# Optimization experiments

Hardware: AMD Instinct MI355X
Metric: run time of the kernel (lower is better)

## Reference

```python
import jax, jax.numpy as jnp
import numpy as np

B, S, QD, KD, VD, OD = 8, 2048, 768, 768, 768, 512

def setup_inputs() -> dict:
    key = jax.random.key(0)
    ks = jax.random.split(key, 14)
    s_q = 1.0 / np.sqrt(QD)
    s_k = 1.0 / np.sqrt(KD)
    s_v = 1.0 / np.sqrt(VD)
    return {
        "query": jax.random.normal(ks[0], (B, S, QD), jnp.float32),
        "key": jax.random.normal(ks[1], (B, S, KD), jnp.float32),
        "value": jax.random.normal(ks[2], (B, S, VD), jnp.float32),
        "Wqr": jax.random.normal(ks[3], (QD, OD), jnp.float32) * s_q,
        "bqr": jnp.zeros((OD,), jnp.float32),
        "Wqi": jax.random.normal(ks[4], (QD, OD), jnp.float32) * s_q,
        "bqi": jnp.zeros((OD,), jnp.float32),
        "Wkr": jax.random.normal(ks[5], (KD, OD), jnp.float32) * s_k,
        "bkr": jnp.zeros((OD,), jnp.float32),
        "Wki": jax.random.normal(ks[6], (KD, OD), jnp.float32) * s_k,
        "bki": jnp.zeros((OD,), jnp.float32),
        "Wv": jax.random.normal(ks[7], (VD, OD), jnp.float32) * s_v,
        "bv": jnp.zeros((OD,), jnp.float32),
        "coherence_weight": jnp.asarray(1.0, jnp.float32),
    }

def reference(query, key, value, Wqr, bqr, Wqi, bqi, Wkr, bkr, Wki, bki, Wv, bv, coherence_weight):
    # Complex-valued projections (real/imag parts via separate linears)
    q_r = jnp.einsum("bsq,qo->bso", query, Wqr) + bqr
    q_i = jnp.einsum("bsq,qo->bso", query, Wqi) + bqi
    k_r = jnp.einsum("bsk,ko->bso", key, Wkr) + bkr
    k_i = jnp.einsum("bsk,ko->bso", key, Wki) + bki
    v = jnp.einsum("bsv,vo->bso", value, Wv) + bv
    # Complex QK^T: (q_r + i q_i)(k_r - i k_i)^T pieces, as in the torch code
    att_real = jnp.einsum("bso,bto->bst", q_r, k_r) + jnp.einsum("bso,bto->bst", q_i, k_i)
    att_imag = jnp.einsum("bso,bto->bst", q_i, k_r) - jnp.einsum("bso,bto->bst", q_r, k_i)
    att_mag = jnp.sqrt(att_real ** 2 + att_imag ** 2)
    scale = jnp.asarray(1.0 / np.sqrt(OD), att_mag.dtype)
    weights = jax.nn.softmax(att_mag * scale, axis=-1)  # [B,S,S]
    output = jnp.einsum("bst,bto->bso", weights, v)  # [B,S,OD]
    coherence = jnp.mean(att_imag ** 2) * coherence_weight
    return output, coherence
```

## Files before the change

kernel.cpp:

```cpp
#include <hip/hip_runtime.h>
#include <math.h>
#include <stdint.h>

#define S_    2048
#define SCALE_ 0.044194173824159216f

typedef __attribute__((ext_vector_type(8))) short short8;
typedef __attribute__((ext_vector_type(4))) float f32x4;

#define MFMA16(a, b, c) __builtin_amdgcn_mfma_f32_16x16x32_bf16((a), (b), (c), 0, 0, 0)

__device__ __forceinline__ void glds16(const void* g, void* l) {
  __builtin_amdgcn_global_load_lds(
      (const __attribute__((address_space(1))) void*)g,
      (__attribute__((address_space(3))) void*)l, 16, 0, 0);
}

__device__ __forceinline__ unsigned short f2bf(float f) {
  unsigned u = __float_as_uint(f);
  u += 0x7FFFu + ((u >> 16) & 1u);
  return (unsigned short)(u >> 16);
}

__global__ __launch_bounds__(256) void convert3_kernel(
    const float* __restrict__ a, const float* __restrict__ b,
    const float* __restrict__ c, unsigned short* __restrict__ oa,
    unsigned short* __restrict__ ob, unsigned short* __restrict__ oc) {
  int i = blockIdx.x * 256 + threadIdx.x;
  int which = i / 3145728;
  int off = i - which * 3145728;
  const float* s = (which == 0) ? a : (which == 1) ? b : c;
  unsigned short* d = (which == 0) ? oa : (which == 1) ? ob : oc;
  float4 v = ((const float4*)s)[off];
  ushort4 o;
  o.x = f2bf(v.x); o.y = f2bf(v.y); o.z = f2bf(v.z); o.w = f2bf(v.w);
  ((ushort4*)d)[off] = o;
}

__global__ void bias_build_kernel(const float* bqr, const float* bqi,
                                  const float* bkr, const float* bki,
                                  const float* bv, float* bq, float* bk,
                                  float* bvo) {
  int t = blockIdx.x * 256 + threadIdx.x;
  if (t < 512) { bq[t] = bqr[t]; bk[t] = bkr[t]; bvo[t] = bv[t]; }
  else if (t < 1024) { bq[t] = bqi[t - 512]; bk[t] = bki[t - 512]; }
}

__global__ __launch_bounds__(256) void wtrans_kernel(
    const float* __restrict__ W, unsigned short* __restrict__ Wt, int N,
    int row_off) {
  __shared__ float t[32][33];
  int n0 = blockIdx.x * 32, k0 = blockIdx.y * 32;
  int tx = threadIdx.x & 31, ty = threadIdx.x >> 5;
#pragma unroll
  for (int r = 0; r < 4; ++r)
    t[ty + r * 8][tx] = W[(size_t)(k0 + ty + r * 8) * N + n0 + tx];
  __syncthreads();
#pragma unroll
  for (int r = 0; r < 4; ++r)
    Wt[(size_t)(row_off + n0 + ty + r * 8) * 768 + k0 + tx] =
        f2bf(t[tx][ty + r * 8]);
}

__global__ void init_kernel(float* lsum, float* coh) {
  int t = blockIdx.x * 256 + threadIdx.x;
  if (t < 16384) lsum[t] = 0.f;
  if (t == 0) *coh = 0.f;
}

__global__ __launch_bounds__(256, 2) void proj_kernel(
    const unsigned short* __restrict__ Xb, const unsigned short* __restrict__ Wt,
    const float* __restrict__ bias, unsigned short* __restrict__ Y, int N,
    int vt_mode) {
  __shared__ char lds[32768];
  const int tid = threadIdx.x;
  const int lane = tid & 63, wid = tid >> 6;
  const int wi = wid >> 1, wj = wid & 1;
  const int m0 = blockIdx.y * 128, n0 = blockIdx.x * 128;
  const char* Xc = (const char*)Xb;
  const char* Wc = (const char*)Wt;

  f32x4 acc[4][4] = {};
  const int tile = wid >> 1;

  for (int s = 0; s < 12; ++s) {
    __syncthreads();
#pragma unroll
    for (int iss = 0; iss < 8; ++iss) {
      int gbase = wid * 512 + iss * 64;
      int loc = (gbase & 1023) + lane;
      int r = loc >> 3, blk = loc & 7;
      int sb = blk ^ (r & 7);
      const char* src = (tile == 0)
          ? Xc + (size_t)(m0 + r) * 1536 + s * 128 + sb * 16
          : Wc + (size_t)(n0 + r) * 1536 + s * 128 + sb * 16;
      glds16(src, lds + gbase * 16);
    }
    __syncthreads();
#pragma unroll
    for (int kk = 0; kk < 2; ++kk) {
      int blk = kk * 4 + (lane >> 4);
      short8 a[4];
#pragma unroll
      for (int i = 0; i < 4; ++i) {
        int row = wi * 64 + i * 16 + (lane & 15);
        a[i] = *(const short8*)(lds + row * 128 + ((blk ^ (row & 7)) << 4));
      }
#pragma unroll
      for (int j = 0; j < 4; ++j) {
        int row = wj * 64 + j * 16 + (lane & 15);
        short8 b = *(const short8*)(lds + 16384 + row * 128 +
                                    ((blk ^ (row & 7)) << 4));
#pragma unroll
        for (int i = 0; i < 4; ++i) acc[i][j] = MFMA16(a[i], b, acc[i][j]);
      }
    }
  }

#pragma unroll
  for (int j = 0; j < 4; ++j) {
    int n = n0 + wj * 64 + j * 16 + (lane & 15);
    float bn = bias[n];
    if (!vt_mode) {
#pragma unroll
      for (int i = 0; i < 4; ++i) {
        int mrow = m0 + wi * 64 + i * 16 + (lane >> 4) * 4;
#pragma unroll
        for (int r = 0; r < 4; ++r)
          Y[(size_t)(mrow + r) * N + n] = f2bf(acc[i][j][r] + bn);
      }
    } else {
#pragma unroll
      for (int i = 0; i < 4; ++i) {
        int mrow = m0 + wi * 64 + i * 16 + (lane >> 4) * 4;
        int b = mrow >> 11, key = mrow & 2047;
        ushort4 o;
        o.x = f2bf(acc[i][j][0] + bn);
        o.y = f2bf(acc[i][j][1] + bn);
        o.z = f2bf(acc[i][j][2] + bn);
        o.w = f2bf(acc[i][j][3] + bn);
        *(ushort4*)&Y[((size_t)b * 512 + n) * 2048 + key] = o;
      }
    }
  }
}

__global__ __launch_bounds__(512, 2) void score_kernel(
    const unsigned short* __restrict__ Qcat,
    const unsigned short* __restrict__ Kcat, unsigned short* __restrict__ P,
    float* __restrict__ lsum, float* __restrict__ coh) {
  __shared__ char lds[147456];
  const int tid = threadIdx.x;
  const int lane = tid & 63, wid = tid >> 6;
  const int wm = wid >> 1;
  const int wn = wid & 1;
  const int lr = lane & 15;
  const int lk = lane >> 4;
  const int l8 = lane >> 3, lb = lane & 7;

  const int id = blockIdx.x;
  const int batch = id & 7;
  const int tile = id >> 3;
  const int q0 = (tile >> 4) << 8;
  const int k0 = (tile & 15) << 7;

  const char* Qc = (const char*)Qcat + ((size_t)batch * 2048 + q0) * 2048;
  const char* Kc = (const char*)Kcat + ((size_t)batch * 2048 + k0) * 2048;

  f32x4 accre[4][4] = {}, accim[4][4] = {};
  const short sg = (short)0x8000;
  const short8 SGN = {sg, sg, sg, sg, sg, sg, sg, sg};

  auto stage = [&](int t, char* setbase, int L) {
    int row, sb;
    const char* src;
    if (L < 32) {
      row = (L << 3) + l8;
      sb = lb ^ (row & 7);
      src = Qc + (size_t)row * 2048 + t * 64 + (sb & 3) * 16 + (sb >> 2) * 1024;
    } else {
      row = ((L - 32) << 3) + l8;
      sb = lb ^ (row & 7);
      src = Kc + (size_t)row * 2048 + t * 64 + (sb & 3) * 16 + (sb >> 2) * 1024;
    }
    glds16(src, setbase + (L << 10));
  };

#pragma unroll
  for (int u = 0; u < 6; ++u) stage(0, lds, wid * 6 + u);
#pragma unroll
  for (int u = 0; u < 6; ++u) stage(1, lds + 49152, wid * 6 + u);
  asm volatile("s_waitcnt vmcnt(6)" ::: "memory");
  __builtin_amdgcn_s_barrier();

  for (int t = 0; t < 16; ++t) {
    char* rbase = lds + (t % 3) * 49152;
    char* wbase = lds + ((t + 2) % 3) * 49152;
    short8 alo[4], ahi[4];
#pragma unroll
    for (int j = 0; j < 4; ++j) {
      if (j == 0) {
#pragma unroll
        for (int i = 0; i < 4; ++i) {
          int ar = wm * 64 + i * 16 + lr;
          const char* arow = rbase + ar * 128;
          alo[i] = *(const short8*)(arow + ((lk ^ (ar & 7)) << 4));
          ahi[i] = *(const short8*)(arow + (((4 + lk) ^ (ar & 7)) << 4));
        }
      }
      int br = wn * 64 + j * 16 + lr;
      const char* brow = rbase + 32768 + br * 128;
      short8 blo = *(const short8*)(brow + ((lk ^ (br & 7)) << 4));
      short8 bhi = *(const short8*)(brow + (((4 + lk) ^ (br & 7)) << 4));
      if (t < 14) {
        if (j == 0)      { stage(t + 2, wbase, wid * 6 + 0); stage(t + 2, wbase, wid * 6 + 1); }
        else if (j == 1) { stage(t + 2, wbase, wid * 6 + 2); stage(t + 2, wbase, wid * 6 + 3); }
        else if (j == 2) { stage(t + 2, wbase, wid * 6 + 4); }
        else             { stage(t + 2, wbase, wid * 6 + 5); }
      }
      __builtin_amdgcn_s_barrier();
      asm volatile("s_waitcnt lgkmcnt(0)" ::: "memory");
      __builtin_amdgcn_sched_barrier(0);
      __builtin_amdgcn_s_setprio(1);
      short8 bhin = bhi ^ SGN;
#pragma unroll
      for (int i = 0; i < 4; ++i) {
        accre[i][j] = MFMA16(alo[i], blo, accre[i][j]);
        accre[i][j] = MFMA16(ahi[i], bhi, accre[i][j]);
        accim[i][j] = MFMA16(ahi[i], blo, accim[i][j]);
        accim[i][j] = MFMA16(alo[i], bhin, accim[i][j]);
      }
      __builtin_amdgcn_s_setprio(0);
      if (j == 3) {
        if (t < 14)       asm volatile("s_waitcnt vmcnt(6)" ::: "memory");
        else if (t == 14) asm volatile("s_waitcnt vmcnt(0)" ::: "memory");
      }
      __builtin_amdgcn_s_barrier();
    }
  }
  __syncthreads();

  float csum = 0.f;
  size_t prow_base = (size_t)batch * 2048;
  float rsum[16];
#pragma unroll
  for (int x = 0; x < 16; ++x) rsum[x] = 0.f;

#pragma unroll
  for (int i = 0; i < 4; ++i) {
#pragma unroll
    for (int r = 0; r < 4; ++r) {
      int row = q0 + wm * 64 + i * 16 + lk * 4 + r;
      unsigned short* prow = P + (prow_base + row) * 2048;
      float rs = 0.f;
#pragma unroll
      for (int j = 0; j < 4; ++j) {
        float re = accre[i][j][r], im = accim[i][j][r];
        csum += im * im;
        float p = __expf(sqrtf(re * re + im * im) * SCALE_);
        rs += p;
        prow[k0 + wn * 64 + j * 16 + lr] = f2bf(p);
      }
      rsum[i * 4 + r] = rs;
    }
  }
#pragma unroll
  for (int x = 0; x < 16; ++x) {
    float v = rsum[x];
    v += __shfl_xor(v, 1, 64);
    v += __shfl_xor(v, 2, 64);
    v += __shfl_xor(v, 4, 64);
    v += __shfl_xor(v, 8, 64);
    rsum[x] = v;
  }
  if (lr == 0) {
#pragma unroll
    for (int i = 0; i < 4; ++i)
#pragma unroll
      for (int r = 0; r < 4; ++r) {
        int row = q0 + wm * 64 + i * 16 + lk * 4 + r;
        atomicAdd(&lsum[prow_base + row], rsum[i * 4 + r]);
      }
  }
#pragma unroll
  for (int m = 1; m < 64; m <<= 1) csum += __shfl_xor(csum, m, 64);
  float* cred = (float*)lds;
  if (lane == 0) cred[wid] = csum;
  __syncthreads();
  if (tid == 0) {
    float s = 0.f;
#pragma unroll
    for (int w = 0; w < 8; ++w) s += cred[w];
    atomicAdd(coh, s);
  }
}

__global__ __launch_bounds__(256, 2) void pv_kernel(
    const unsigned short* __restrict__ P, const unsigned short* __restrict__ Vt,
    const float* __restrict__ lsum, float* __restrict__ out) {
  __shared__ char lds[32768];
  const int tid = threadIdx.x;
  const int lane = tid & 63, wid = tid >> 6;
  const int wi = wid >> 1, wj = wid & 1;

  int id = blockIdx.x;
  int w = (id & 7) * 64 + (id >> 3);
  int batch = w >> 6, tilein = w & 63;
  int i0 = (tilein >> 2) * 128;
  int o0 = (tilein & 3) * 128;

  const char* Pc = (const char*)P + (size_t)batch * 2048 * 4096;
  const char* Vc = (const char*)Vt + (size_t)batch * 512 * 4096;

  f32x4 acc[4][4] = {};
  const int tile = wid >> 1;

  for (int s = 0; s < 32; ++s) {
    __syncthreads();
#pragma unroll
    for (int iss = 0; iss < 8; ++iss) {
      int gbase = wid * 512 + iss * 64;
      int loc = (gbase & 1023) + lane;
      int r = loc >> 3, blk = loc & 7;
      int sb = blk ^ (r & 7);
      const char* src = (tile == 0)
          ? Pc + (size_t)(i0 + r) * 4096 + s * 128 + sb * 16
          : Vc + (size_t)(o0 + r) * 4096 + s * 128 + sb * 16;
      glds16(src, lds + gbase * 16);
    }
    __syncthreads();
#pragma unroll
    for (int kk = 0; kk < 2; ++kk) {
      int blk = kk * 4 + (lane >> 4);
      short8 a[4];
#pragma unroll
      for (int i = 0; i < 4; ++i) {
        int row = wi * 64 + i * 16 + (lane & 15);
        a[i] = *(const short8*)(lds + row * 128 + ((blk ^ (row & 7)) << 4));
      }
#pragma unroll
      for (int j = 0; j < 4; ++j) {
        int row = wj * 64 + j * 16 + (lane & 15);
        short8 b = *(const short8*)(lds + 16384 + row * 128 +
                                    ((blk ^ (row & 7)) << 4));
#pragma unroll
        for (int i = 0; i < 4; ++i) acc[i][j] = MFMA16(a[i], b, acc[i][j]);
      }
    }
  }

#pragma unroll
  for (int i = 0; i < 4; ++i) {
    int mrow = i0 + wi * 64 + i * 16 + (lane >> 4) * 4;
    float linv[4];
#pragma unroll
    for (int r = 0; r < 4; ++r)
      linv[r] = 1.0f / lsum[(size_t)batch * 2048 + mrow + r];
#pragma unroll
    for (int j = 0; j < 4; ++j) {
      int n = o0 + wj * 64 + j * 16 + (lane & 15);
#pragma unroll
      for (int r = 0; r < 4; ++r)
        out[((size_t)batch * 2048 + mrow + r) * 512 + n] = acc[i][j][r] * linv[r];
    }
  }
}

__global__ void finalize_kernel(const float* __restrict__ coh,
                                const float* __restrict__ cw,
                                float* __restrict__ out_last) {
  *out_last = (*coh) * (1.0f / 33554432.0f) * (*cw);
}

extern "C" void kernel_launch(void* const* d_in, const int* in_sizes, int n_in,
                              void* d_out, int out_size, void* d_ws,
                              size_t ws_size, hipStream_t stream) {
  const float* query = (const float*)d_in[0];
  const float* key   = (const float*)d_in[1];
  const float* value = (const float*)d_in[2];
  const float* Wqr = (const float*)d_in[3];
  const float* bqr = (const float*)d_in[4];
  const float* Wqi = (const float*)d_in[5];
  const float* bqi = (const float*)d_in[6];
  const float* Wkr = (const float*)d_in[7];
  const float* bkr = (const float*)d_in[8];
  const float* Wki = (const float*)d_in[9];
  const float* bki = (const float*)d_in[10];
  const float* Wv  = (const float*)d_in[11];
  const float* bv  = (const float*)d_in[12];
  const float* cw  = (const float*)d_in[13];
  float* out = (float*)d_out;

  char* ws = (char*)d_ws;
  unsigned short* XQ   = (unsigned short*)(ws + 0);
  unsigned short* XK   = (unsigned short*)(ws + 25165824);
  unsigned short* XV   = (unsigned short*)(ws + 50331648);
  unsigned short* Pbuf = (unsigned short*)(ws + 0);
  unsigned short* WTQ  = (unsigned short*)(ws + 75497472);
  unsigned short* WTK  = (unsigned short*)(ws + 77070336);
  unsigned short* WTV  = (unsigned short*)(ws + 78643200);
  float* BQ   = (float*)(ws + 79429632);
  float* BK   = (float*)(ws + 79433728);
  float* BV   = (float*)(ws + 79437824);
  unsigned short* QCAT = (unsigned short*)(ws + 79441920);
  unsigned short* KCAT = (unsigned short*)(ws + 112996352);
  unsigned short* VT   = (unsigned short*)(ws + 146550784);
  float* LSUM = (float*)(ws + 163328000);
  float* COH  = (float*)(ws + 163393536);
  if (ws_size < 163393600) return;

  convert3_kernel<<<36864, 256, 0, stream>>>(query, key, value, XQ, XK, XV);
  bias_build_kernel<<<4, 256, 0, stream>>>(bqr, bqi, bkr, bki, bv, BQ, BK, BV);
  wtrans_kernel<<<dim3(16, 24), 256, 0, stream>>>(Wqr, WTQ, 512, 0);
  wtrans_kernel<<<dim3(16, 24), 256, 0, stream>>>(Wqi, WTQ, 512, 512);
  wtrans_kernel<<<dim3(16, 24), 256, 0, stream>>>(Wkr, WTK, 512, 0);
  wtrans_kernel<<<dim3(16, 24), 256, 0, stream>>>(Wki, WTK, 512, 512);
  wtrans_kernel<<<dim3(16, 24), 256, 0, stream>>>(Wv, WTV, 512, 0);

  proj_kernel<<<dim3(8, 128), 256, 0, stream>>>(XQ, WTQ, BQ, QCAT, 1024, 0);
  proj_kernel<<<dim3(8, 128), 256, 0, stream>>>(XK, WTK, BK, KCAT, 1024, 0);
  proj_kernel<<<dim3(4, 128), 256, 0, stream>>>(XV, WTV, BV, VT, 512, 1);

  init_kernel<<<64, 256, 0, stream>>>(LSUM, COH);
  score_kernel<<<1024, 512, 0, stream>>>(QCAT, KCAT, Pbuf, LSUM, COH);
  pv_kernel<<<512, 256, 0, stream>>>(Pbuf, VT, LSUM, out);
  finalize_kernel<<<1, 1, 0, stream>>>(COH, cw, out + 8388608);
}
```

Baseline: 383.3 us.

## Double-buffer proj/pv loads and enlarge score tile to 256x256

Proj and pv kernels now double-buffer their LDS tiles, issuing the next K-step's global-to-LDS loads before computing the current one, and precompute source pointers outside the loop. The score kernel changes from 256x128 tiles with a triple-buffered fine-grained pipeline to 256x256 tiles with a simple double buffer, 8x4 accumulators per wave, and half as many blocks. The goal is to hide load latency and raise data reuse per block. In exchange, score occupancy drops to one block per CU with much higher register pressure. The hand-tuned setprio and waitcnt scheduling is also dropped.

Result: slower. 1.523 ms (+297.5%).

```diff
diff --git a/kernel.cpp b/kernel.cpp
--- a/kernel.cpp
+++ b/kernel.cpp
@@ -72,31 +72,43 @@
     const unsigned short* __restrict__ Xb, const unsigned short* __restrict__ Wt,
     const float* __restrict__ bias, unsigned short* __restrict__ Y, int N,
     int vt_mode) {
-  __shared__ char lds[32768];
+  __shared__ char lds[65536];
   const int tid = threadIdx.x;
   const int lane = tid & 63, wid = tid >> 6;
   const int wi = wid >> 1, wj = wid & 1;
   const int m0 = blockIdx.y * 128, n0 = blockIdx.x * 128;
   const char* Xc = (const char*)Xb;
   const char* Wc = (const char*)Wt;
+  const int tile = wid >> 1;
+
+  const char* sp[8];
+  int sd[8];
+#pragma unroll
+  for (int iss = 0; iss < 8; ++iss) {
+    int gbase = wid * 512 + iss * 64;
+    int loc = (gbase & 1023) + lane;
+    int r = loc >> 3, blk = loc & 7;
+    int sb = blk ^ (r & 7);
+    sp[iss] = (tile == 0) ? Xc + (size_t)(m0 + r) * 1536 + sb * 16
+                          : Wc + (size_t)(n0 + r) * 1536 + sb * 16;
+    sd[iss] = gbase * 16;
+  }
 
   f32x4 acc[4][4] = {};
-  const int tile = wid >> 1;
-
+
+#pragma unroll
+  for (int iss = 0; iss < 8; ++iss) glds16(sp[iss], lds + sd[iss]);
+
+#pragma unroll 2
   for (int s = 0; s < 12; ++s) {
     __syncthreads();
-#pragma unroll
-    for (int iss = 0; iss < 8; ++iss) {
-      int gbase = wid * 512 + iss * 64;
-      int loc = (gbase & 1023) + lane;
-      int r = loc >> 3, blk = loc & 7;
-      int sb = blk ^ (r & 7);
-      const char* src = (tile == 0)
-          ? Xc + (size_t)(m0 + r) * 1536 + s * 128 + sb * 16
-          : Wc + (size_t)(n0 + r) * 1536 + s * 128 + sb * 16;
-      glds16(src, lds + gbase * 16);
-    }
-    __syncthreads();
+    if (s + 1 < 12) {
+      char* wb = lds + ((s + 1) & 1) * 32768;
+#pragma unroll
+      for (int iss = 0; iss < 8; ++iss)
+        glds16(sp[iss] + (s + 1) * 128, wb + sd[iss]);
+    }
+    char* rb = lds + (s & 1) * 32768;
 #pragma unroll
     for (int kk = 0; kk < 2; ++kk) {
       int blk = kk * 4 + (lane >> 4);
@@ -104,12 +116,12 @@
 #pragma unroll
       for (int i = 0; i < 4; ++i) {
         int row = wi * 64 + i * 16 + (lane & 15);
-        a[i] = *(const short8*)(lds + row * 128 + ((blk ^ (row & 7)) << 4));
+        a[i] = *(const short8*)(rb + row * 128 + ((blk ^ (row & 7)) << 4));
       }
 #pragma unroll
       for (int j = 0; j < 4; ++j) {
         int row = wj * 64 + j * 16 + (lane & 15);
-        short8 b = *(const short8*)(lds + 16384 + row * 128 +
+        short8 b = *(const short8*)(rb + 16384 + row * 128 +
                                     ((blk ^ (row & 7)) << 4));
 #pragma unroll
         for (int i = 0; i < 4; ++i) acc[i][j] = MFMA16(a[i], b, acc[i][j]);
@@ -145,15 +157,15 @@
   }
 }
 
-__global__ __launch_bounds__(512, 2) void score_kernel(
+__global__ __launch_bounds__(512, 1) void score_kernel(
     const unsigned short* __restrict__ Qcat,
     const unsigned short* __restrict__ Kcat, unsigned short* __restrict__ P,
     float* __restrict__ lsum, float* __restrict__ coh) {
-  __shared__ char lds[147456];
+  __shared__ char lds[131072];
   const int tid = threadIdx.x;
   const int lane = tid & 63, wid = tid >> 6;
-  const int wm = wid >> 1;
-  const int wn = wid & 1;
+  const int wm = wid >> 2;
+  const int wn = wid & 3;
   const int lr = lane & 15;
   const int lk = lane >> 4;
   const int l8 = lane >> 3, lb = lane & 7;
@@ -161,96 +173,83 @@
   const int id = blockIdx.x;
   const int batch = id & 7;
   const int tile = id >> 3;
-  const int q0 = (tile >> 4) << 8;
-  const int k0 = (tile & 15) << 7;
+  const int q0 = (tile >> 3) << 8;
+  const int k0 = (tile & 7) << 8;
 
   const char* Qc = (const char*)Qcat + ((size_t)batch * 2048 + q0) * 2048;
   const char* Kc = (const char*)Kcat + ((size_t)batch * 2048 + k0) * 2048;
 
-  f32x4 accre[4][4] = {}, accim[4][4] = {};
+  const char* sp[8];
+  int sd[8];
+#pragma unroll
+  for (int u = 0; u < 8; ++u) {
+    int L = wid * 8 + u;
+    int row = ((L & 31) << 3) + l8;
+    int sb = lb ^ (row & 7);
+    const char* base = (L < 32) ? Qc : Kc;
+    sp[u] = base + (size_t)row * 2048 + (sb & 3) * 16 + (sb >> 2) * 1024;
+    sd[u] = L << 10;
+  }
+
+  int aoff_lo[8], aoff_hi[8], boff_lo[4], boff_hi[4];
+#pragma unroll
+  for (int i = 0; i < 8; ++i) {
+    int ar = wm * 128 + i * 16 + lr;
+    aoff_lo[i] = ar * 128 + ((lk ^ (ar & 7)) << 4);
+    aoff_hi[i] = ar * 128 + (((4 + lk) ^ (ar & 7)) << 4);
+  }
+#pragma unroll
+  for (int j = 0; j < 4; ++j) {
+    int br = wn * 64 + j * 16 + lr;
+    boff_lo[j] = 32768 + br * 128 + ((lk ^ (br & 7)) << 4);
+    boff_hi[j] = 32768 + br * 128 + (((4 + lk) ^ (br & 7)) << 4);
+  }
+
+  f32x4 accre[8][4] = {}, accim[8][4] = {};
   const short sg = (short)0x8000;
   const short8 SGN = {sg, sg, sg, sg, sg, sg, sg, sg};
 
-  auto stage = [&](int t, char* setbase, int L) {
-    int row, sb;
-    const char* src;
-    if (L < 32) {
-      row = (L << 3) + l8;
-      sb = lb ^ (row & 7);
-      src = Qc + (size_t)row * 2048 + t * 64 + (sb & 3) * 16 + (sb >> 2) * 1024;
-    } else {
-      row = ((L - 32) << 3) + l8;
-      sb = lb ^ (row & 7);
-      src = Kc + (size_t)row * 2048 + t * 64 + (sb & 3) * 16 + (sb >> 2) * 1024;
-    }
-    glds16(src, setbase + (L << 10));
-  };
-
-#pragma unroll
-  for (int u = 0; u < 6; ++u) stage(0, lds, wid * 6 + u);
-#pragma unroll
-  for (int u = 0; u < 6; ++u) stage(1, lds + 49152, wid * 6 + u);
-  asm volatile("s_waitcnt vmcnt(6)" ::: "memory");
-  __builtin_amdgcn_s_barrier();
-
+#pragma unroll
+  for (int u = 0; u < 8; ++u) glds16(sp[u], lds + sd[u]);
+
+#pragma unroll 2
   for (int t = 0; t < 16; ++t) {
-    char* rbase = lds + (t % 3) * 49152;
-    char* wbase = lds + ((t + 2) % 3) * 49152;
-    short8 alo[4], ahi[4];
+    __syncthreads();
+    if (t + 1 < 16) {
+      char* wb = lds + ((t + 1) & 1) * 65536;
+#pragma unroll
+      for (int u = 0; u < 8; ++u)
+        glds16(sp[u] + (t + 1) * 64, wb + sd[u]);
+    }
+    const char* rb = lds + (t & 1) * 65536;
+    short8 alo[8], ahi[8];
+#pragma unroll
+    for (int i = 0; i < 8; ++i) {
+      alo[i] = *(const short8*)(rb + aoff_lo[i]);
+      ahi[i] = *(const short8*)(rb + aoff_hi[i]);
+    }
 #pragma unroll
     for (int j = 0; j < 4; ++j) {
-      if (j == 0) {
-#pragma unroll
-        for (int i = 0; i < 4; ++i) {
-          int ar = wm * 64 + i * 16 + lr;
-          const char* arow = rbase + ar * 128;
-          alo[i] = *(const short8*)(arow + ((lk ^ (ar & 7)) << 4));
-          ahi[i] = *(const short8*)(arow + (((4 + lk) ^ (ar & 7)) << 4));
-        }
-      }
-      int br = wn * 64 + j * 16 + lr;
-      const char* brow = rbase + 32768 + br * 128;
-      short8 blo = *(const short8*)(brow + ((lk ^ (br & 7)) << 4));
-      short8 bhi = *(const short8*)(brow + (((4 + lk) ^ (br & 7)) << 4));
-      if (t < 14) {
-        if (j == 0)      { stage(t + 2, wbase, wid * 6 + 0); stage(t + 2, wbase, wid * 6 + 1); }
-        else if (j == 1) { stage(t + 2, wbase, wid * 6 + 2); stage(t + 2, wbase, wid * 6 + 3); }
-        else if (j == 2) { stage(t + 2, wbase, wid * 6 + 4); }
-        else             { stage(t + 2, wbase, wid * 6 + 5); }
-      }
-      __builtin_amdgcn_s_barrier();
-      asm volatile("s_waitcnt lgkmcnt(0)" ::: "memory");
-      __builtin_amdgcn_sched_barrier(0);
-      __builtin_amdgcn_s_setprio(1);
+      short8 blo = *(const short8*)(rb + boff_lo[j]);
+      short8 bhi = *(const short8*)(rb + boff_hi[j]);
       short8 bhin = bhi ^ SGN;
 #pragma unroll
-      for (int i = 0; i < 4; ++i) {
+      for (int i = 0; i < 8; ++i) {
         accre[i][j] = MFMA16(alo[i], blo, accre[i][j]);
         accre[i][j] = MFMA16(ahi[i], bhi, accre[i][j]);
         accim[i][j] = MFMA16(ahi[i], blo, accim[i][j]);
         accim[i][j] = MFMA16(alo[i], bhin, accim[i][j]);
       }
-      __builtin_amdgcn_s_setprio(0);
-      if (j == 3) {
-        if (t < 14)       asm volatile("s_waitcnt vmcnt(6)" ::: "memory");
-        else if (t == 14) asm volatile("s_waitcnt vmcnt(0)" ::: "memory");
-      }
-      __builtin_amdgcn_s_barrier();
-    }
-  }
-  __syncthreads();
+    }
+  }
 
   float csum = 0.f;
   size_t prow_base = (size_t)batch * 2048;
-  float rsum[16];
-#pragma unroll
-  for (int x = 0; x < 16; ++x) rsum[x] = 0.f;
-
-#pragma unroll
-  for (int i = 0; i < 4; ++i) {
+#pragma unroll
+  for (int i = 0; i < 8; ++i) {
 #pragma unroll
     for (int r = 0; r < 4; ++r) {
-      int row = q0 + wm * 64 + i * 16 + lk * 4 + r;
+      int row = q0 + wm * 128 + i * 16 + lk * 4 + r;
       unsigned short* prow = P + (prow_base + row) * 2048;
       float rs = 0.f;
 #pragma unroll
@@ -261,26 +260,12 @@
         rs += p;
         prow[k0 + wn * 64 + j * 16 + lr] = f2bf(p);
       }
-      rsum[i * 4 + r] = rs;
-    }
-  }
-#pragma unroll
-  for (int x = 0; x < 16; ++x) {
-    float v = rsum[x];
-    v += __shfl_xor(v, 1, 64);
-    v += __shfl_xor(v, 2, 64);
-    v += __shfl_xor(v, 4, 64);
-    v += __shfl_xor(v, 8, 64);
-    rsum[x] = v;
-  }
-  if (lr == 0) {
-#pragma unroll
-    for (int i = 0; i < 4; ++i)
-#pragma unroll
-      for (int r = 0; r < 4; ++r) {
-        int row = q0 + wm * 64 + i * 16 + lk * 4 + r;
-        atomicAdd(&lsum[prow_base + row], rsum[i * 4 + r]);
-      }
+      rs += __shfl_xor(rs, 1, 64);
+      rs += __shfl_xor(rs, 2, 64);
+      rs += __shfl_xor(rs, 4, 64);
+      rs += __shfl_xor(rs, 8, 64);
+      if (lr == 0) atomicAdd(&lsum[prow_base + row], rs);
+    }
   }
 #pragma unroll
   for (int m = 1; m < 64; m <<= 1) csum += __shfl_xor(csum, m, 64);
@@ -298,7 +283,7 @@
 __global__ __launch_bounds__(256, 2) void pv_kernel(
     const unsigned short* __restrict__ P, const unsigned short* __restrict__ Vt,
     const float* __restrict__ lsum, float* __restrict__ out) {
-  __shared__ char lds[32768];
+  __shared__ char lds[65536];
   const int tid = threadIdx.x;
   const int lane = tid & 63, wid = tid >> 6;
   const int wi = wid >> 1, wj = wid & 1;
@@ -311,24 +296,36 @@
 
   const char* Pc = (const char*)P + (size_t)batch * 2048 * 4096;
   const char* Vc = (const char*)Vt + (size_t)batch * 512 * 4096;
+  const int tile = wid >> 1;
+
+  const char* sp[8];
+  int sd[8];
+#pragma unroll
+  for (int iss = 0; iss < 8; ++iss) {
+    int gbase = wid * 512 + iss * 64;
+    int loc = (gbase & 1023) + lane;
+    int r = loc >> 3, blk = loc & 7;
+    int sb = blk ^ (r & 7);
+    sp[iss] = (tile == 0) ? Pc + (size_t)(i0 + r) * 4096 + sb * 16
+                          : Vc + (size_t)(o0 + r) * 4096 + sb * 16;
+    sd[iss] = gbase * 16;
+  }
 
   f32x4 acc[4][4] = {};
-  const int tile = wid >> 1;
-
+
+#pragma unroll
+  for (int iss = 0; iss < 8; ++iss) glds16(sp[iss], lds + sd[iss]);
+
+#pragma unroll 2
   for (int s = 0; s < 32; ++s) {
     __syncthreads();
-#pragma unroll
-    for (int iss = 0; iss < 8; ++iss) {
-      int gbase = wid * 512 + iss * 64;
-      int loc = (gbase & 1023) + lane;
-      int r = loc >> 3, blk = loc & 7;
-      int sb = blk ^ (r & 7);
-      const char* src = (tile == 0)
-          ? Pc + (size_t)(i0 + r) * 4096 + s * 128 + sb * 16
-          : Vc + (size_t)(o0 + r) * 4096 + s * 128 + sb * 16;
-      glds16(src, lds + gbase * 16);
-    }
-    __syncthreads();
+    if (s + 1 < 32) {
+      char* wb = lds + ((s + 1) & 1) * 32768;
+#pragma unroll
+      for (int iss = 0; iss < 8; ++iss)
+        glds16(sp[iss] + (s + 1) * 128, wb + sd[iss]);
+    }
+    char* rb = lds + (s & 1) * 32768;
 #pragma unroll
     for (int kk = 0; kk < 2; ++kk) {
       int blk = kk * 4 + (lane >> 4);
@@ -336,12 +333,12 @@
 #pragma unroll
       for (int i = 0; i < 4; ++i) {
         int row = wi * 64 + i * 16 + (lane & 15);
-        a[i] = *(const short8*)(lds + row * 128 + ((blk ^ (row & 7)) << 4));
+        a[i] = *(const short8*)(rb + row * 128 + ((blk ^ (row & 7)) << 4));
       }
 #pragma unroll
       for (int j = 0; j < 4; ++j) {
         int row = wj * 64 + j * 16 + (lane & 15);
-        short8 b = *(const short8*)(lds + 16384 + row * 128 +
+        short8 b = *(const short8*)(rb + 16384 + row * 128 +
                                     ((blk ^ (row & 7)) << 4));
 #pragma unroll
         for (int i = 0; i < 4; ++i) acc[i][j] = MFMA16(a[i], b, acc[i][j]);
@@ -422,7 +419,7 @@
   proj_kernel<<<dim3(4, 128), 256, 0, stream>>>(XV, WTV, BV, VT, 512, 1);
 
   init_kernel<<<64, 256, 0, stream>>>(LSUM, COH);
-  score_kernel<<<1024, 512, 0, stream>>>(QCAT, KCAT, Pbuf, LSUM, COH);
+  score_kernel<<<512, 512, 0, stream>>>(QCAT, KCAT, Pbuf, LSUM, COH);
   pv_kernel<<<512, 256, 0, stream>>>(Pbuf, VT, LSUM, out);
   finalize_kernel<<<1, 1, 0, stream>>>(COH, cw, out + 8388608);
 }
```

## Simplify score kernel pipeline to double-buffered LDS with one barrier per step

Applied to the files above, without the earlier changes.

Replaces the triple-buffered, finely interleaved prefetch schedule (per-j barriers, manual waitcnt, setprio) in the score kernel with a plain double buffer. Each k-step now has a single __syncthreads and issues the next tile's global-to-LDS loads up front. Global and LDS addresses are precomputed, LDS drops from 144KB to 96KB, and launch bounds go to one block per SM. The row-sum reduction is also done per row inline. The intent is fewer barriers and less address arithmetic, but prefetch distance shrinks to one stage and the explicit wait/priority control is lost, so load latency may be exposed.

After: 361.9 us. -5.6%, faster.

```diff
diff --git a/kernel.cpp b/kernel.cpp
--- a/kernel.cpp
+++ b/kernel.cpp
@@ -145,11 +145,11 @@
   }
 }
 
-__global__ __launch_bounds__(512, 2) void score_kernel(
+__global__ __launch_bounds__(512, 1) void score_kernel(
     const unsigned short* __restrict__ Qcat,
     const unsigned short* __restrict__ Kcat, unsigned short* __restrict__ P,
     float* __restrict__ lsum, float* __restrict__ coh) {
-  __shared__ char lds[147456];
+  __shared__ char lds[98304];
   const int tid = threadIdx.x;
   const int lane = tid & 63, wid = tid >> 6;
   const int wm = wid >> 1;
@@ -167,61 +167,59 @@
   const char* Qc = (const char*)Qcat + ((size_t)batch * 2048 + q0) * 2048;
   const char* Kc = (const char*)Kcat + ((size_t)batch * 2048 + k0) * 2048;
 
+  const char* sp[6];
+  int sd[6];
+#pragma unroll
+  for (int u = 0; u < 6; ++u) {
+    int L = wid * 6 + u;
+    int row = ((L & 31) << 3) + l8;
+    int sb = lb ^ (row & 7);
+    const char* base = (L < 32) ? Qc : Kc;
+    sp[u] = base + (size_t)row * 2048 + (sb & 3) * 16 + (sb >> 2) * 1024;
+    sd[u] = L << 10;
+  }
+
+  int aoff_lo[4], aoff_hi[4], boff_lo[4], boff_hi[4];
+#pragma unroll
+  for (int i = 0; i < 4; ++i) {
+    int ar = wm * 64 + i * 16 + lr;
+    aoff_lo[i] = ar * 128 + ((lk ^ (ar & 7)) << 4);
+    aoff_hi[i] = ar * 128 + (((4 + lk) ^ (ar & 7)) << 4);
+  }
+#pragma unroll
+  for (int j = 0; j < 4; ++j) {
+    int br = wn * 64 + j * 16 + lr;
+    boff_lo[j] = 32768 + br * 128 + ((lk ^ (br & 7)) << 4);
+    boff_hi[j] = 32768 + br * 128 + (((4 + lk) ^ (br & 7)) << 4);
+  }
+
   f32x4 accre[4][4] = {}, accim[4][4] = {};
   const short sg = (short)0x8000;
   const short8 SGN = {sg, sg, sg, sg, sg, sg, sg, sg};
 
-  auto stage = [&](int t, char* setbase, int L) {
-    int row, sb;
-    const char* src;
-    if (L < 32) {
-      row = (L << 3) + l8;
-      sb = lb ^ (row & 7);
-      src = Qc + (size_t)row * 2048 + t * 64 + (sb & 3) * 16 + (sb >> 2) * 1024;
-    } else {
-      row = ((L - 32) << 3) + l8;
-      sb = lb ^ (row & 7);
-      src = Kc + (size_t)row * 2048 + t * 64 + (sb & 3) * 16 + (sb >> 2) * 1024;
-    }
-    glds16(src, setbase + (L << 10));
-  };
-
-#pragma unroll
-  for (int u = 0; u < 6; ++u) stage(0, lds, wid * 6 + u);
-#pragma unroll
-  for (int u = 0; u < 6; ++u) stage(1, lds + 49152, wid * 6 + u);
-  asm volatile("s_waitcnt vmcnt(6)" ::: "memory");
-  __builtin_amdgcn_s_barrier();
-
+#pragma unroll
+  for (int u = 0; u < 6; ++u) glds16(sp[u], lds + sd[u]);
+
+#pragma unroll 2
   for (int t = 0; t < 16; ++t) {
-    char* rbase = lds + (t % 3) * 49152;
-    char* wbase = lds + ((t + 2) % 3) * 49152;
+    __syncthreads();
+    if (t + 1 < 16) {
+      char* wb = lds + ((t + 1) & 1) * 49152;
+#pragma unroll
+      for (int u = 0; u < 6; ++u)
+        glds16(sp[u] + (t + 1) * 64, wb + sd[u]);
+    }
+    const char* rb = lds + (t & 1) * 49152;
     short8 alo[4], ahi[4];
 #pragma unroll
+    for (int i = 0; i < 4; ++i) {
+      alo[i] = *(const short8*)(rb + aoff_lo[i]);
+      ahi[i] = *(const short8*)(rb + aoff_hi[i]);
+    }
+#pragma unroll
     for (int j = 0; j < 4; ++j) {
-      if (j == 0) {
-#pragma unroll
-        for (int i = 0; i < 4; ++i) {
-          int ar = wm * 64 + i * 16 + lr;
-          const char* arow = rbase + ar * 128;
-          alo[i] = *(const short8*)(arow + ((lk ^ (ar & 7)) << 4));
-          ahi[i] = *(const short8*)(arow + (((4 + lk) ^ (ar & 7)) << 4));
-        }
-      }
-      int br = wn * 64 + j * 16 + lr;
-      const char* brow = rbase + 32768 + br * 128;
-      short8 blo = *(const short8*)(brow + ((lk ^ (br & 7)) << 4));
-      short8 bhi = *(const short8*)(brow + (((4 + lk) ^ (br & 7)) << 4));
-      if (t < 14) {
-        if (j == 0)      { stage(t + 2, wbase, wid * 6 + 0); stage(t + 2, wbase, wid * 6 + 1); }
-        else if (j == 1) { stage(t + 2, wbase, wid * 6 + 2); stage(t + 2, wbase, wid * 6 + 3); }
-        else if (j == 2) { stage(t + 2, wbase, wid * 6 + 4); }
-        else             { stage(t + 2, wbase, wid * 6 + 5); }
-      }
-      __builtin_amdgcn_s_barrier();
-      asm volatile("s_waitcnt lgkmcnt(0)" ::: "memory");
-      __builtin_amdgcn_sched_barrier(0);
-      __builtin_amdgcn_s_setprio(1);
+      short8 blo = *(const short8*)(rb + boff_lo[j]);
+      short8 bhi = *(const short8*)(rb + boff_hi[j]);
       short8 bhin = bhi ^ SGN;
 #pragma unroll
       for (int i = 0; i < 4; ++i) {
@@ -230,22 +228,11 @@
         accim[i][j] = MFMA16(ahi[i], blo, accim[i][j]);
         accim[i][j] = MFMA16(alo[i], bhin, accim[i][j]);
       }
-      __builtin_amdgcn_s_setprio(0);
-      if (j == 3) {
-        if (t < 14)       asm volatile("s_waitcnt vmcnt(6)" ::: "memory");
-        else if (t == 14) asm volatile("s_waitcnt vmcnt(0)" ::: "memory");
-      }
-      __builtin_amdgcn_s_barrier();
-    }
-  }
-  __syncthreads();
+    }
+  }
 
   float csum = 0.f;
   size_t prow_base = (size_t)batch * 2048;
-  float rsum[16];
-#pragma unroll
-  for (int x = 0; x < 16; ++x) rsum[x] = 0.f;
-
 #pragma unroll
   for (int i = 0; i < 4; ++i) {
 #pragma unroll
@@ -261,30 +248,17 @@
         rs += p;
         prow[k0 + wn * 64 + j * 16 + lr] = f2bf(p);
       }
-      rsum[i * 4 + r] = rs;
-    }
-  }
-#pragma unroll
-  for (int x = 0; x < 16; ++x) {
-    float v = rsum[x];
-    v += __shfl_xor(v, 1, 64);
-    v += __shfl_xor(v, 2, 64);
-    v += __shfl_xor(v, 4, 64);
-    v += __shfl_xor(v, 8, 64);
-    rsum[x] = v;
-  }
-  if (lr == 0) {
-#pragma unroll
-    for (int i = 0; i < 4; ++i)
-#pragma unroll
-      for (int r = 0; r < 4; ++r) {
-        int row = q0 + wm * 64 + i * 16 + lk * 4 + r;
-        atomicAdd(&lsum[prow_base + row], rsum[i * 4 + r]);
-      }
+      rs += __shfl_xor(rs, 1, 64);
+      rs += __shfl_xor(rs, 2, 64);
+      rs += __shfl_xor(rs, 4, 64);
+      rs += __shfl_xor(rs, 8, 64);
+      if (lr == 0) atomicAdd(&lsum[prow_base + row], rs);
+    }
   }
 #pragma unroll
   for (int m = 1; m < 64; m <<= 1) csum += __shfl_xor(csum, m, 64);
   float* cred = (float*)lds;
+  __syncthreads();
   if (lane == 0) cred[wid] = csum;
   __syncthreads();
   if (tid == 0) {
```
